# Performance work log

Measured on AMD Instinct MI355X. Metric: run time of the kernel, lower is better.

The kernel has to match this reference:

```python
import jax, jax.numpy as jnp
import numpy as np

N_NODES = 100000
N_EDGES = 1200000
NODE_DIM = 128
HIDDEN = 64
N_POSTS = 50000


def setup_inputs() -> dict:
    key = jax.random.key(0)
    ks = jax.random.split(key, 10)
    s = 1.0 / np.sqrt(NODE_DIM)
    sh = 1.0 / np.sqrt(HIDDEN)
    return {
        "node_features": jax.random.normal(ks[0], (N_NODES, NODE_DIM), dtype=jnp.float32),
        "edge_index": jax.random.randint(ks[1], (2, N_EDGES), 0, N_NODES, dtype=jnp.int64) if jax.config.jax_enable_x64 else jax.random.randint(ks[1], (2, N_EDGES), 0, N_NODES, dtype=jnp.int32),
        "post_mask": jax.random.randint(ks[2], (N_POSTS,), 0, N_NODES, dtype=jnp.int32),
        "W_enc": jax.random.uniform(ks[3], (NODE_DIM, HIDDEN), jnp.float32, -s, s),
        "b_enc": jax.random.uniform(ks[4], (HIDDEN,), jnp.float32, -s, s),
        "W_conv": jax.random.uniform(ks[5], (HIDDEN, HIDDEN), jnp.float32, -sh, sh),
        "b_conv": jax.random.uniform(ks[6], (HIDDEN,), jnp.float32, -sh, sh),
        "W_out": jax.random.uniform(ks[7], (HIDDEN, 1), jnp.float32, -sh, sh),
        "b_out": jax.random.uniform(ks[8], (1,), jnp.float32, -sh, sh),
    }


def reference(node_features, edge_index, post_mask, W_enc, b_enc, W_conv, b_conv, W_out, b_out):
    # encode: relu(Linear)
    node_emb = jax.nn.relu(node_features @ W_enc + b_enc)  # [N, H]
    src, dst = edge_index[0], edge_index[1]
    # per-edge gather then scatter-add into destination nodes (segment sum)
    messages = jax.ops.segment_sum(node_emb[src], dst, num_segments=node_emb.shape[0])  # [N, H]
    node_emb = jax.nn.relu((node_emb + messages) @ W_conv + b_conv)  # [N, H]
    post_emb = node_emb[post_mask]  # [P, H]
    out = jax.nn.sigmoid((post_emb @ W_out + b_out).squeeze(-1))  # [P]
    return out
```

## Files before the change

kernel.cpp:

```cpp
#include <hip/hip_runtime.h>
#include <hip/hip_bf16.h>
#include <math.h>


#define HIDDEN 64
#define NODE_DIM 128
#define SCAN_CHUNK 1024

typedef __attribute__((ext_vector_type(8))) short short8;
typedef __attribute__((ext_vector_type(4))) float floatx4;

union F2B { short8 s; __hip_bfloat162 h[4]; };

__device__ inline short8 cvt8(const float4& p, const float4& q) {
    F2B u;
    u.h[0] = __float22bfloat162_rn(make_float2(p.x, p.y));
    u.h[1] = __float22bfloat162_rn(make_float2(p.z, p.w));
    u.h[2] = __float22bfloat162_rn(make_float2(q.x, q.y));
    u.h[3] = __float22bfloat162_rn(make_float2(q.z, q.w));
    return u.s;
}

__device__ inline void cvt8_split(const float4& p, const float4& q,
                                  short8& hi, short8& lo) {
    const float f[8] = {p.x, p.y, p.z, p.w, q.x, q.y, q.z, q.w};
    F2B uh, ul;
    #pragma unroll
    for (int jj = 0; jj < 4; ++jj) {
        const float2 v = make_float2(f[2 * jj], f[2 * jj + 1]);
        const __hip_bfloat162 h = __float22bfloat162_rn(v);
        const float2 hv = __bfloat1622float2(h);
        ul.h[jj] = __float22bfloat162_rn(make_float2(v.x - hv.x, v.y - hv.y));
        uh.h[jj] = h;
    }
    hi = uh.s; lo = ul.s;
}

__global__ __launch_bounds__(256) void k_pre(
    const int* __restrict__ post, unsigned int* __restrict__ bits,
    int* __restrict__ nodelist, int* __restrict__ listCnt,
    int* __restrict__ count, int n_posts, int n_nodes)
{
    const int gtid = blockIdx.x * 256 + threadIdx.x;
    if (gtid < n_nodes) count[gtid] = 0;
    if (gtid < n_posts) {
        const int n = post[gtid];
        const unsigned int bit = 1u << (n & 31);
        const unsigned int old = atomicOr(&bits[n >> 5], bit);
        if (!(old & bit)) {
            const int i = atomicAdd(listCnt, 1);
            nodelist[i] = n;
        }
    }
}

__global__ __launch_bounds__(256) void k_encode_count(
    const float* __restrict__ A, const float* __restrict__ We,
    const float* __restrict__ be, __hip_bfloat16* __restrict__ emb16,
    const int* __restrict__ dsts, const unsigned int* __restrict__ bits,
    int* __restrict__ count, int n_nodes, int n_tiles, int n_edges)
{
    __shared__ float sWe[NODE_DIM * HIDDEN];

    {
        const float4* src = (const float4*)We;
        float4* dst = (float4*)sWe;
        #pragma unroll
        for (int i = 0; i < (NODE_DIM * HIDDEN / 4) / 256; ++i)
            dst[i * 256 + threadIdx.x] = src[i * 256 + threadIdx.x];
    }
    __syncthreads();

    const int lane = threadIdx.x & 63;
    const int r    = lane & 15;
    const int quad = lane >> 4;

    short8 Wb[4][4];
    #pragma unroll
    for (int ks = 0; ks < 4; ++ks)
        #pragma unroll
        for (int nt = 0; nt < 4; ++nt) {
            F2B u;
            #pragma unroll
            for (int jj = 0; jj < 4; ++jj) {
                const int k0 = ks * 32 + quad * 8 + 2 * jj;
                const float lo = sWe[k0 * HIDDEN + nt * 16 + r];
                const float hi = sWe[(k0 + 1) * HIDDEN + nt * 16 + r];
                u.h[jj] = __float22bfloat162_rn(make_float2(lo, hi));
            }
            Wb[ks][nt] = u.s;
        }
    float bias[4];
    #pragma unroll
    for (int nt = 0; nt < 4; ++nt) bias[nt] = be[nt * 16 + r];

    const int wid    = (blockIdx.x * 256 + threadIdx.x) >> 6;
    const int nwaves = gridDim.x * 4;

    int t = wid;
    float4 a[4][2];
    if (t < n_tiles) {
        const float* Arow = A + (size_t)t * 16 * NODE_DIM + (size_t)r * NODE_DIM + quad * 8;
        #pragma unroll
        for (int ks = 0; ks < 4; ++ks) {
            a[ks][0] = *(const float4*)(Arow + ks * 32);
            a[ks][1] = *(const float4*)(Arow + ks * 32 + 4);
        }
    }
    while (t < n_tiles) {
        const int tn = t + nwaves;
        float4 b[4][2];
        #pragma unroll
        for (int ks = 0; ks < 4; ++ks) {
            b[ks][0] = make_float4(0.f, 0.f, 0.f, 0.f);
            b[ks][1] = make_float4(0.f, 0.f, 0.f, 0.f);
        }
        if (tn < n_tiles) {
            const float* Brow = A + (size_t)tn * 16 * NODE_DIM + (size_t)r * NODE_DIM + quad * 8;
            #pragma unroll
            for (int ks = 0; ks < 4; ++ks) {
                b[ks][0] = *(const float4*)(Brow + ks * 32);
                b[ks][1] = *(const float4*)(Brow + ks * 32 + 4);
            }
        }
        floatx4 acc[4] = {};
        #pragma unroll
        for (int ks = 0; ks < 4; ++ks) {
            const short8 af = cvt8(a[ks][0], a[ks][1]);
            #pragma unroll
            for (int nt = 0; nt < 4; ++nt)
                acc[nt] = __builtin_amdgcn_mfma_f32_16x16x32_bf16(af, Wb[ks][nt], acc[nt], 0, 0, 0);
        }
        #pragma unroll
        for (int nt = 0; nt < 4; ++nt)
            #pragma unroll
            for (int g = 0; g < 4; ++g) {
                const int node = t * 16 + quad * 4 + g;
                const float h = fmaxf(acc[nt][g] + bias[nt], 0.0f);
                emb16[(size_t)node * HIDDEN + nt * 16 + r] = __float2bfloat16(h);
            }
        #pragma unroll
        for (int ks = 0; ks < 4; ++ks) {
            a[ks][0] = b[ks][0];
            a[ks][1] = b[ks][1];
        }
        t = tn;
    }
    const int rem = n_nodes - n_tiles * 16;
    if (rem > 0 && wid == 0) {
        for (int n = n_tiles * 16; n < n_nodes; ++n) {
            float acc = be[lane];
            const float* row = A + (size_t)n * NODE_DIM;
            for (int k = 0; k < NODE_DIM; ++k)
                acc = fmaf(row[k], We[(size_t)k * HIDDEN + lane], acc);
            emb16[(size_t)n * HIDDEN + lane] = __float2bfloat16(fmaxf(acc, 0.0f));
        }
    }

    const int stride = gridDim.x * 256;
    for (int e = blockIdx.x * 256 + threadIdx.x; e < n_edges; e += stride) {
        const int d = dsts[e];
        if ((bits[d >> 5] >> (d & 31)) & 1u) atomicAdd(&count[d], 1);
    }
}

__global__ __launch_bounds__(256) void k_scan_lb(
    const int* __restrict__ count, int* __restrict__ row_start,
    unsigned int* __restrict__ partials, int n)
{
    __shared__ int s[256];
    __shared__ int sExc;
    const int b = blockIdx.x, tid = threadIdx.x;
    const int base = b * SCAN_CHUNK + tid * 4;
    int c0 = (base + 0 < n) ? count[base + 0] : 0;
    int c1 = (base + 1 < n) ? count[base + 1] : 0;
    int c2 = (base + 2 < n) ? count[base + 2] : 0;
    int c3 = (base + 3 < n) ? count[base + 3] : 0;
    const int t = c0 + c1 + c2 + c3;
    s[tid] = t;
    __syncthreads();
    #pragma unroll
    for (int off = 1; off < 256; off <<= 1) {
        int v = (tid >= off) ? s[tid - off] : 0;
        __syncthreads();
        s[tid] += v;
        __syncthreads();
    }
    const int total = s[255];

    if (b == 0) {
        if (tid == 0) {
            __hip_atomic_store(&partials[0], (2u << 30) | (unsigned int)total,
                               __ATOMIC_RELEASE, __HIP_MEMORY_SCOPE_AGENT);
            sExc = 0;
        }
    } else {
        if (tid == 0) {
            __hip_atomic_store(&partials[b], (1u << 30) | (unsigned int)total,
                               __ATOMIC_RELEASE, __HIP_MEMORY_SCOPE_AGENT);
        }
        if (tid < 64) {
            int exc = 0;
            int winEnd = b;
            while (true) {
                const int j = winEnd - 64 + tid;
                const unsigned int v = (j >= 0)
                    ? __hip_atomic_load(&partials[j], __ATOMIC_ACQUIRE,
                                        __HIP_MEMORY_SCOPE_AGENT)
                    : (2u << 30);
                const unsigned int st = v >> 30;
                if (__ballot(st == 0u)) {
                    __builtin_amdgcn_s_sleep(1);
                    continue;
                }
                const unsigned long long b2 = __ballot(st == 2u);
                int contrib;
                bool done;
                if (b2) {
                    const int hi = 63 - __clzll(b2);
                    contrib = (tid >= hi) ? (int)(v & 0x3FFFFFFFu) : 0;
                    done = true;
                } else {
                    contrib = (int)(v & 0x3FFFFFFFu);
                    done = false;
                }
                #pragma unroll
                for (int off = 1; off < 64; off <<= 1)
                    contrib += __shfl_xor(contrib, off);
                exc += contrib;
                if (done) break;
                winEnd -= 64;
            }
            if (tid == 0) {
                __hip_atomic_store(&partials[b],
                                   (2u << 30) | (unsigned int)(exc + total),
                                   __ATOMIC_RELEASE, __HIP_MEMORY_SCOPE_AGENT);
                sExc = exc;
            }
        }
    }
    __syncthreads();
    int run = sExc + s[tid] - t;
    if (base + 0 < n) row_start[base + 0] = run;           run += c0;
    if (base + 1 < n) row_start[base + 1] = run;           run += c1;
    if (base + 2 < n) row_start[base + 2] = run;           run += c2;
    if (base + 3 < n) row_start[base + 3] = run;
}

__global__ __launch_bounds__(256) void k_fill(
    const int* __restrict__ srcs, const int* __restrict__ dsts,
    const unsigned int* __restrict__ bits, int* __restrict__ row_start,
    int* __restrict__ slots, int n_edges)
{
    const int stride = gridDim.x * 256;
    for (int e = blockIdx.x * 256 + threadIdx.x; e < n_edges; e += stride) {
        const int d = dsts[e];
        if (!((bits[d >> 5] >> (d & 31)) & 1u)) continue;
        const int idx = atomicAdd(&row_start[d], 1);
        slots[idx] = srcs[e];
    }
}

__global__ __launch_bounds__(256) void k_gather(
    const int* __restrict__ nodelist, const int* __restrict__ listCnt,
    const int* __restrict__ row_end, const int* __restrict__ count,
    const int* __restrict__ slots, const __hip_bfloat16* __restrict__ emb16,
    float* __restrict__ msg_c)
{
    const int lane = threadIdx.x & 63;
    const int j    = lane & 7;
    const int g    = lane >> 3;
    const int gw   = (blockIdx.x * 256 + threadIdx.x) >> 6;
    const int nw   = gridDim.x * 4;
    const int nc   = listCnt[0];

    for (int i = gw; i < nc; i += nw) {
        const int n    = nodelist[i];
        const int m    = count[n];
        const int base = row_end[n] - m;

        float2 a0 = {0.f, 0.f}, a1 = {0.f, 0.f}, a2 = {0.f, 0.f}, a3 = {0.f, 0.f};
        #define ACC8(v)  do { F2B u; u.s = (v); float2 t;                       \
            t = __bfloat1622float2(u.h[0]); a0.x += t.x; a0.y += t.y;           \
            t = __bfloat1622float2(u.h[1]); a1.x += t.x; a1.y += t.y;           \
            t = __bfloat1622float2(u.h[2]); a2.x += t.x; a2.y += t.y;           \
            t = __bfloat1622float2(u.h[3]); a3.x += t.x; a3.y += t.y; } while (0)

        if (g == 0) {
            const short8 v = *(const short8*)(emb16 + (size_t)n * HIDDEN + j * 8);
            ACC8(v);
        }
        int c = g;
        for (; c + 8 < m; c += 16) {
            const int s0 = slots[base + c];
            const int s1 = slots[base + c + 8];
            const short8 v0 = *(const short8*)(emb16 + (size_t)s0 * HIDDEN + j * 8);
            const short8 v1 = *(const short8*)(emb16 + (size_t)s1 * HIDDEN + j * 8);
            ACC8(v0); ACC8(v1);
        }
        for (; c < m; c += 8) {
            const int s0 = slots[base + c];
            const short8 v0 = *(const short8*)(emb16 + (size_t)s0 * HIDDEN + j * 8);
            ACC8(v0);
        }
        #undef ACC8

        #pragma unroll
        for (int off = 8; off < 64; off <<= 1) {
            a0.x += __shfl_xor(a0.x, off); a0.y += __shfl_xor(a0.y, off);
            a1.x += __shfl_xor(a1.x, off); a1.y += __shfl_xor(a1.y, off);
            a2.x += __shfl_xor(a2.x, off); a2.y += __shfl_xor(a2.y, off);
            a3.x += __shfl_xor(a3.x, off); a3.y += __shfl_xor(a3.y, off);
        }
        if (g == 0) {
            float4* dst = (float4*)(msg_c + (size_t)i * HIDDEN + j * 8);
            dst[0] = make_float4(a0.x, a0.y, a1.x, a1.y);
            dst[1] = make_float4(a2.x, a2.y, a3.x, a3.y);
        }
    }
}

__global__ __launch_bounds__(256) void k_head_mfma(
    const int* __restrict__ listCnt, const int* __restrict__ nodelist,
    const float* __restrict__ msg_c,
    const float* __restrict__ Wc, const float* __restrict__ bc,
    const float* __restrict__ Wo, const float* __restrict__ bo,
    float* __restrict__ res)
{
    const int lane = threadIdx.x & 63;
    const int r    = lane & 15;
    const int quad = lane >> 4;

    short8 Wb[2][4];
    #pragma unroll
    for (int ks = 0; ks < 2; ++ks)
        #pragma unroll
        for (int nt = 0; nt < 4; ++nt) {
            F2B u;
            #pragma unroll
            for (int jj = 0; jj < 4; ++jj) {
                const int k0 = ks * 32 + quad * 8 + 2 * jj;
                const float lo = Wc[(size_t)k0 * HIDDEN + nt * 16 + r];
                const float hi = Wc[(size_t)(k0 + 1) * HIDDEN + nt * 16 + r];
                u.h[jj] = __float22bfloat162_rn(make_float2(lo, hi));
            }
            Wb[ks][nt] = u.s;
        }
    float bias[4], wo[4];
    #pragma unroll
    for (int nt = 0; nt < 4; ++nt) { bias[nt] = bc[nt * 16 + r]; wo[nt] = Wo[nt * 16 + r]; }
    const float bo_s = bo[0];

    const int nc      = listCnt[0];
    const int n_tiles = (nc + 15) / 16;
    const int wid     = (blockIdx.x * 256 + threadIdx.x) >> 6;
    const int nwaves  = gridDim.x * 4;

    for (int tile = wid; tile < n_tiles; tile += nwaves) {
        const int i0  = tile * 16;
        const int row = i0 + r;
        floatx4 acc[4] = {};
        #pragma unroll
        for (int ks = 0; ks < 2; ++ks) {
            float4 f0 = make_float4(0.f, 0.f, 0.f, 0.f), f1 = f0;
            if (row < nc) {
                const float* src = msg_c + (size_t)row * HIDDEN + ks * 32 + quad * 8;
                f0 = *(const float4*)src;
                f1 = *(const float4*)(src + 4);
            }
            short8 ah, al;
            cvt8_split(f0, f1, ah, al);
            #pragma unroll
            for (int nt = 0; nt < 4; ++nt) {
                acc[nt] = __builtin_amdgcn_mfma_f32_16x16x32_bf16(ah, Wb[ks][nt], acc[nt], 0, 0, 0);
                acc[nt] = __builtin_amdgcn_mfma_f32_16x16x32_bf16(al, Wb[ks][nt], acc[nt], 0, 0, 0);
            }
        }
        float r4[4];
        #pragma unroll
        for (int gg = 0; gg < 4; ++gg) {
            float part = 0.0f;
            #pragma unroll
            for (int nt = 0; nt < 4; ++nt)
                part += fmaxf(acc[nt][gg] + bias[nt], 0.0f) * wo[nt];
            part += __shfl_xor(part, 1);
            part += __shfl_xor(part, 2);
            part += __shfl_xor(part, 4);
            part += __shfl_xor(part, 8);
            r4[gg] = part;
        }
        if (r == 0) {
            #pragma unroll
            for (int gg = 0; gg < 4; ++gg) {
                const int idx = i0 + quad * 4 + gg;
                if (idx < nc)
                    res[nodelist[idx]] = 1.0f / (1.0f + __expf(-(r4[gg] + bo_s)));
            }
        }
    }
}

__global__ __launch_bounds__(256) void k_out(
    const int* __restrict__ post, const float* __restrict__ res,
    float* __restrict__ out, int n_posts)
{
    const int p = blockIdx.x * 256 + threadIdx.x;
    if (p < n_posts) out[p] = res[post[p]];
}

extern "C" void kernel_launch(void* const* d_in, const int* in_sizes, int n_in,
                              void* d_out, int out_size, void* d_ws, size_t ws_size,
                              hipStream_t stream) {
    const float* A    = (const float*)d_in[0];
    const int*   ei   = (const int*)  d_in[1];
    const int*   post = (const int*)  d_in[2];
    const float* We   = (const float*)d_in[3];
    const float* be   = (const float*)d_in[4];
    const float* Wc   = (const float*)d_in[5];
    const float* bc   = (const float*)d_in[6];
    const float* Wo   = (const float*)d_in[7];
    const float* bo   = (const float*)d_in[8];
    float* out = (float*)d_out;

    const int n_nodes = in_sizes[0] / NODE_DIM;
    const int n_edges = in_sizes[1] / 2;
    const int n_posts = in_sizes[2];

    char* p = (char*)d_ws;
    __hip_bfloat16* emb16 = (__hip_bfloat16*)p;  p += (size_t)n_nodes * HIDDEN * 2;
    float* msg_c    = (float*)p;              p += (size_t)n_posts * HIDDEN * 4;
    int*   slots    = (int*)p;                p += (size_t)n_edges * 4;
    char* zbase = p;
    unsigned int* bits = (unsigned int*)p;    p += ((size_t)(n_nodes + 31) / 32 + 32) * 4;
    int*   listCnt  = (int*)p;                p += 256;
    unsigned int* partials = (unsigned int*)p; p += 1024;
    const size_t zbytes = (size_t)(p - zbase);
    int*   count    = (int*)p;                p += (size_t)n_nodes * 4;
    int*   row_start= (int*)p;                p += (size_t)n_nodes * 4;
    int*   nodelist = (int*)p;                p += (size_t)n_nodes * 4;
    float* res      = (float*)p;              p += (size_t)n_nodes * 4;

    const int* srcs = ei;
    const int* dsts = ei + n_edges;
    const int nb = (n_nodes + SCAN_CHUNK - 1) / SCAN_CHUNK;
    const int n_tiles = n_nodes / 16;

    hipMemsetAsync(zbase, 0, zbytes, stream);
    k_pre<<<(n_nodes + 255) / 256, 256, 0, stream>>>(post, bits, nodelist, listCnt, count, n_posts, n_nodes);
    k_encode_count<<<512, 256, 0, stream>>>(A, We, be, emb16, dsts, bits, count, n_nodes, n_tiles, n_edges);
    k_scan_lb<<<nb, 256, 0, stream>>>(count, row_start, partials, n_nodes);
    k_fill<<<2048, 256, 0, stream>>>(srcs, dsts, bits, row_start, slots, n_edges);
    k_gather<<<8192, 256, 0, stream>>>(nodelist, listCnt, row_start, count, slots, emb16, msg_c);
    k_head_mfma<<<1024, 256, 0, stream>>>(listCnt, nodelist, msg_c, Wc, bc, Wo, bo, res);
    k_out<<<(n_posts + 255) / 256, 256, 0, stream>>>(post, res, out, n_posts);
}
```

Before: 201.3 us.

## Record edge ranks during counting and assign one 8-lane group per post node

```diff
diff --git a/kernel.cpp b/kernel.cpp
--- a/kernel.cpp
+++ b/kernel.cpp
@@ -58,7 +58,8 @@
     const float* __restrict__ A, const float* __restrict__ We,
     const float* __restrict__ be, __hip_bfloat16* __restrict__ emb16,
     const int* __restrict__ dsts, const unsigned int* __restrict__ bits,
-    int* __restrict__ count, int n_nodes, int n_tiles, int n_edges)
+    int* __restrict__ count, int* __restrict__ rank,
+    int n_nodes, int n_tiles, int n_edges)
 {
     __shared__ float sWe[NODE_DIM * HIDDEN];
 
@@ -160,7 +161,8 @@
     const int stride = gridDim.x * 256;
     for (int e = blockIdx.x * 256 + threadIdx.x; e < n_edges; e += stride) {
         const int d = dsts[e];
-        if ((bits[d >> 5] >> (d & 31)) & 1u) atomicAdd(&count[d], 1);
+        if ((bits[d >> 5] >> (d & 31)) & 1u)
+            rank[e] = atomicAdd(&count[d], 1);
     }
 }
 
@@ -249,35 +251,34 @@
 
 __global__ __launch_bounds__(256) void k_fill(
     const int* __restrict__ srcs, const int* __restrict__ dsts,
-    const unsigned int* __restrict__ bits, int* __restrict__ row_start,
-    int* __restrict__ slots, int n_edges)
+    const unsigned int* __restrict__ bits, const int* __restrict__ row_start,
+    const int* __restrict__ rank, int* __restrict__ slots, int n_edges)
 {
     const int stride = gridDim.x * 256;
     for (int e = blockIdx.x * 256 + threadIdx.x; e < n_edges; e += stride) {
         const int d = dsts[e];
         if (!((bits[d >> 5] >> (d & 31)) & 1u)) continue;
-        const int idx = atomicAdd(&row_start[d], 1);
-        slots[idx] = srcs[e];
+        slots[row_start[d] + rank[e]] = srcs[e];
     }
 }
 
 __global__ __launch_bounds__(256) void k_gather(
     const int* __restrict__ nodelist, const int* __restrict__ listCnt,
-    const int* __restrict__ row_end, const int* __restrict__ count,
+    const int* __restrict__ row_start, const int* __restrict__ count,
     const int* __restrict__ slots, const __hip_bfloat16* __restrict__ emb16,
     float* __restrict__ msg_c)
 {
     const int lane = threadIdx.x & 63;
     const int j    = lane & 7;
     const int g    = lane >> 3;
-    const int gw   = (blockIdx.x * 256 + threadIdx.x) >> 6;
-    const int nw   = gridDim.x * 4;
+    const int wavei = (blockIdx.x * 256 + threadIdx.x) >> 6;
+    const int ngroups = gridDim.x * 4 * 8;
     const int nc   = listCnt[0];
 
-    for (int i = gw; i < nc; i += nw) {
+    for (int i = wavei * 8 + g; i < nc; i += ngroups) {
         const int n    = nodelist[i];
         const int m    = count[n];
-        const int base = row_end[n] - m;
+        const int base = row_start[n];
 
         float2 a0 = {0.f, 0.f}, a1 = {0.f, 0.f}, a2 = {0.f, 0.f}, a3 = {0.f, 0.f};
         #define ACC8(v)  do { F2B u; u.s = (v); float2 t;                       \
@@ -286,37 +287,28 @@
             t = __bfloat1622float2(u.h[2]); a2.x += t.x; a2.y += t.y;           \
             t = __bfloat1622float2(u.h[3]); a3.x += t.x; a3.y += t.y; } while (0)
 
-        if (g == 0) {
+        {
             const short8 v = *(const short8*)(emb16 + (size_t)n * HIDDEN + j * 8);
             ACC8(v);
         }
-        int c = g;
-        for (; c + 8 < m; c += 16) {
+        int c = 0;
+        for (; c + 1 < m; c += 2) {
             const int s0 = slots[base + c];
-            const int s1 = slots[base + c + 8];
+            const int s1 = slots[base + c + 1];
             const short8 v0 = *(const short8*)(emb16 + (size_t)s0 * HIDDEN + j * 8);
             const short8 v1 = *(const short8*)(emb16 + (size_t)s1 * HIDDEN + j * 8);
             ACC8(v0); ACC8(v1);
         }
-        for (; c < m; c += 8) {
+        if (c < m) {
             const int s0 = slots[base + c];
             const short8 v0 = *(const short8*)(emb16 + (size_t)s0 * HIDDEN + j * 8);
             ACC8(v0);
         }
         #undef ACC8
 
-        #pragma unroll
-        for (int off = 8; off < 64; off <<= 1) {
-            a0.x += __shfl_xor(a0.x, off); a0.y += __shfl_xor(a0.y, off);
-            a1.x += __shfl_xor(a1.x, off); a1.y += __shfl_xor(a1.y, off);
-            a2.x += __shfl_xor(a2.x, off); a2.y += __shfl_xor(a2.y, off);
-            a3.x += __shfl_xor(a3.x, off); a3.y += __shfl_xor(a3.y, off);
-        }
-        if (g == 0) {
-            float4* dst = (float4*)(msg_c + (size_t)i * HIDDEN + j * 8);
-            dst[0] = make_float4(a0.x, a0.y, a1.x, a1.y);
-            dst[1] = make_float4(a2.x, a2.y, a3.x, a3.y);
-        }
+        float4* dst = (float4*)(msg_c + (size_t)i * HIDDEN + j * 8);
+        dst[0] = make_float4(a0.x, a0.y, a1.x, a1.y);
+        dst[1] = make_float4(a2.x, a2.y, a3.x, a3.y);
     }
 }
 
@@ -430,6 +422,7 @@
     __hip_bfloat16* emb16 = (__hip_bfloat16*)p;  p += (size_t)n_nodes * HIDDEN * 2;
     float* msg_c    = (float*)p;              p += (size_t)n_posts * HIDDEN * 4;
     int*   slots    = (int*)p;                p += (size_t)n_edges * 4;
+    int*   rank     = (int*)p;                p += (size_t)n_edges * 4;
     char* zbase = p;
     unsigned int* bits = (unsigned int*)p;    p += ((size_t)(n_nodes + 31) / 32 + 32) * 4;
     int*   listCnt  = (int*)p;                p += 256;
@@ -447,10 +440,10 @@
 
     hipMemsetAsync(zbase, 0, zbytes, stream);
     k_pre<<<(n_nodes + 255) / 256, 256, 0, stream>>>(post, bits, nodelist, listCnt, count, n_posts, n_nodes);
-    k_encode_count<<<512, 256, 0, stream>>>(A, We, be, emb16, dsts, bits, count, n_nodes, n_tiles, n_edges);
+    k_encode_count<<<512, 256, 0, stream>>>(A, We, be, emb16, dsts, bits, count, rank, n_nodes, n_tiles, n_edges);
     k_scan_lb<<<nb, 256, 0, stream>>>(count, row_start, partials, n_nodes);
-    k_fill<<<2048, 256, 0, stream>>>(srcs, dsts, bits, row_start, slots, n_edges);
-    k_gather<<<8192, 256, 0, stream>>>(nodelist, listCnt, row_start, count, slots, emb16, msg_c);
+    k_fill<<<2048, 256, 0, stream>>>(srcs, dsts, bits, row_start, rank, slots, n_edges);
+    k_gather<<<1024, 256, 0, stream>>>(nodelist, listCnt, row_start, count, slots, emb16, msg_c);
     k_head_mfma<<<1024, 256, 0, stream>>>(listCnt, nodelist, msg_c, Wc, bc, Wo, bo, res);
     k_out<<<(n_posts + 255) / 256, 256, 0, stream>>>(post, res, out, n_posts);
 }
```

Result: faster. 188.2 us (-6.5%).
